# Optimization experiments

Measured on AMD Instinct MI355X. Metric: run time of the kernel, lower is better.

## Reference

```python
import jax, jax.numpy as jnp
import numpy as np

NQ = 8
NL = 3
DIM = 2 ** NQ


def _rx(psi, w, theta):
    # theta: scalar or [B]
    B = psi.shape[0]
    t = jnp.atleast_1d(theta).astype(jnp.float32)
    c = jnp.cos(t / 2)[:, None, None].astype(jnp.complex64)
    s = (-1j * jnp.sin(t / 2))[:, None, None].astype(jnp.complex64)
    p = psi.reshape(B, 2 ** w, 2, -1)
    s0, s1 = p[:, :, 0], p[:, :, 1]
    return jnp.stack([c * s0 + s * s1, s * s0 + c * s1], axis=2).reshape(B, DIM)


def _ry(psi, w, theta):
    B = psi.shape[0]
    t = jnp.atleast_1d(theta).astype(jnp.float32)
    c = jnp.cos(t / 2)[:, None, None].astype(jnp.complex64)
    s = jnp.sin(t / 2)[:, None, None].astype(jnp.complex64)
    p = psi.reshape(B, 2 ** w, 2, -1)
    s0, s1 = p[:, :, 0], p[:, :, 1]
    return jnp.stack([c * s0 - s * s1, s * s0 + c * s1], axis=2).reshape(B, DIM)


def _rz(psi, w, theta):
    B = psi.shape[0]
    t = jnp.atleast_1d(theta).astype(jnp.float32)
    e0 = jnp.exp(-0.5j * t.astype(jnp.complex64))[:, None, None]
    e1 = jnp.exp(0.5j * t.astype(jnp.complex64))[:, None, None]
    p = psi.reshape(B, 2 ** w, 2, -1)
    return jnp.stack([e0 * p[:, :, 0], e1 * p[:, :, 1]], axis=2).reshape(B, DIM)


def _cnot(psi, c, t):
    # control c, target t (wire 0 = most significant axis)
    B = psi.shape[0]
    a, b = (c, t) if c < t else (t, c)
    p = psi.reshape(B, 2 ** a, 2, 2 ** (b - a - 1), 2, -1)
    caxis = 2 if c < t else 4
    taxis = 4 if c < t else 2
    idx = [slice(None)] * 6
    idx[caxis] = 1
    sub = p[tuple(idx)]  # control=1 slab, caxis removed
    fl_axis = taxis - (1 if taxis > caxis else 0)
    p = p.at[tuple(idx)].set(jnp.flip(sub, axis=fl_axis))
    return p.reshape(B, DIM)


# PauliZ signs per wire: [NQ, 2^NQ]
_bits = (np.arange(DIM)[None, :] >> (NQ - 1 - np.arange(NQ)[:, None])) & 1
_Z_SIGNS = jnp.asarray((1 - 2 * _bits).astype(np.float32))


def _quantum_layer(enc, qrx, qry, qrz):
    # enc: [B, NQ] encoding angles; qrx/qry/qrz: [NL, NQ] scalar params
    B = enc.shape[0]
    psi = jnp.zeros((B, DIM), jnp.complex64).at[:, 0].set(1.0)
    for i in range(NQ):
        psi = _rx(psi, i, enc[:, i])
    for l in range(NL):
        for i in range(NQ):
            psi = _rx(psi, i, qrx[l, i])
            psi = _ry(psi, i, qry[l, i])
            psi = _rz(psi, i, qrz[l, i])
        for i in range(NQ - 1):
            psi = _cnot(psi, i, i + 1)
        psi = _cnot(psi, NQ - 1, 0)
    probs = psi.real ** 2 + psi.imag ** 2  # [B, 2^NQ]
    return probs @ _Z_SIGNS.T  # [B, NQ] <Z_i>


def _critic(x, w1, b1, w2, b2, qrx, qry, qrz, w3, b3, w4, b4):
    h = jax.nn.relu(x @ w1 + b1)
    enc = h @ w2 + b2
    ex = _quantum_layer(enc, qrx, qry, qrz)
    h2 = jax.nn.relu(ex @ w3 + b3)
    return h2 @ w4 + b4


def setup_inputs() -> dict:
    key = jax.random.key(0)
    ks = jax.random.split(key, 32)
    B, OBS, ACT, H = 65536, 96, 32, 256
    D = OBS + ACT

    def lin(k, fin, fout):
        return jax.random.normal(k, (fin, fout), jnp.float32) * (1.0 / np.sqrt(fin))

    inp = {
        'state': jax.random.normal(ks[0], (B, OBS), jnp.float32),
        'action': jax.random.normal(ks[1], (B, ACT), jnp.float32),
    }
    for ci, tag in enumerate(['a', 'b']):
        o = 2 + ci * 15
        inp['w1' + tag] = lin(ks[o + 0], D, H)
        inp['b1' + tag] = jnp.zeros((H,), jnp.float32)
        inp['w2' + tag] = lin(ks[o + 1], H, NQ)
        inp['b2' + tag] = jnp.zeros((NQ,), jnp.float32)
        inp['qrx' + tag] = jax.random.normal(ks[o + 2], (NL, NQ), jnp.float32)
        inp['qry' + tag] = jax.random.normal(ks[o + 3], (NL, NQ), jnp.float32)
        inp['qrz' + tag] = jax.random.normal(ks[o + 4], (NL, NQ), jnp.float32)
        inp['w3' + tag] = lin(ks[o + 5], NQ, H)
        inp['b3' + tag] = jnp.zeros((H,), jnp.float32)
        inp['w4' + tag] = lin(ks[o + 6], H, 1)
        inp['b4' + tag] = jnp.zeros((1,), jnp.float32)
    return inp


def reference(state, action,
              w1a, b1a, w2a, b2a, qrxa, qrya, qrza, w3a, b3a, w4a, b4a,
              w1b, b1b, w2b, b2b, qrxb, qryb, qrzb, w3b, b3b, w4b, b4b):
    x = jnp.concatenate([state, action], axis=1)
    q1 = _critic(x, w1a, b1a, w2a, b2a, qrxa, qrya, qrza, w3a, b3a, w4a, b4a)
    q2 = _critic(x, w1b, b1b, w2b, b2b, qrxb, qryb, qrzb, w3b, b3b, w4b, b4b)
    return (q1, q2)
```

## Files before the change

### kernel.cpp

```cpp
#include <hip/hip_runtime.h>
#include <math.h>


typedef __attribute__((ext_vector_type(8))) short bfrag_t;
typedef __attribute__((ext_vector_type(16))) float accv_t;

__device__ __forceinline__ unsigned short f2bf(float x) {
  unsigned u = __float_as_uint(x);
  u += 0x7FFFu + ((u >> 16) & 1u);
  return (unsigned short)(u >> 16);
}
__device__ __forceinline__ float bf2f(unsigned short h) {
  return __uint_as_float(((unsigned)h) << 16);
}
__device__ __forceinline__ unsigned pack2(float a, float b) {
  return (unsigned)f2bf(a) | ((unsigned)f2bf(b) << 16);
}

struct C2 { float r, i; };
__device__ __forceinline__ C2 cmul(C2 a, C2 b){ return C2{a.r*b.r - a.i*b.i, a.r*b.i + a.i*b.r}; }
__device__ __forceinline__ C2 cadd(C2 a, C2 b){ return C2{a.r+b.r, a.i+b.i}; }

#define APPLY2(A,Bx)                                                        \
  { float ar=re[A], ai=im[A], br=re[Bx], bi=im[Bx];                         \
    re[A]  = u00r*ar - u00i*ai + u01r*br - u01i*bi;                         \
    im[A]  = u00r*ai + u00i*ar + u01r*bi + u01i*br;                         \
    re[Bx] = u10r*ar - u10i*ai + u11r*br - u11i*bi;                         \
    im[Bx] = u10r*ai + u10i*ar + u11r*bi + u11i*br; }

__global__ __launch_bounds__(256)
void prep_weights(const float* __restrict__ qrxa, const float* __restrict__ qrya,
                  const float* __restrict__ qrza,
                  const float* __restrict__ qrxb, const float* __restrict__ qryb,
                  const float* __restrict__ qrzb,
                  const float* __restrict__ w1a, const float* __restrict__ w1b,
                  const float* __restrict__ w2a, const float* __restrict__ w2b,
                  const float* __restrict__ w3a, const float* __restrict__ w3b,
                  unsigned short* __restrict__ Bm, unsigned short* __restrict__ Gm,
                  unsigned short* __restrict__ w1p, unsigned short* __restrict__ w2p) {
  int blk = blockIdx.x;
  int tid = threadIdx.x;
  if (blk < 128) {
    __shared__ float sg[192];
    int c = blk >> 6;
    if (tid < 24) {
      const float* qx = c ? qrxb : qrxa;
      const float* qy = c ? qryb : qrya;
      const float* qz = c ? qrzb : qrza;
      int g = tid;
      float tx = 0.5f*qx[g], ty = 0.5f*qy[g], tz = 0.5f*qz[g];
      float cx = cosf(tx), sx = sinf(tx);
      float cy = cosf(ty), sy = sinf(ty);
      float cz = cosf(tz), sz = sinf(tz);
      C2 rx00{cx,0.f}, rx01{0.f,-sx}, rx10{0.f,-sx}, rx11{cx,0.f};
      C2 m00 = cadd(cmul(C2{cy,0.f},rx00), cmul(C2{-sy,0.f},rx10));
      C2 m01 = cadd(cmul(C2{cy,0.f},rx01), cmul(C2{-sy,0.f},rx11));
      C2 m10 = cadd(cmul(C2{sy,0.f},rx00), cmul(C2{cy,0.f},rx10));
      C2 m11 = cadd(cmul(C2{sy,0.f},rx01), cmul(C2{cy,0.f},rx11));
      C2 e0{cz,-sz}, e1{cz,sz};
      C2 u00 = cmul(e0,m00), u01 = cmul(e0,m01), u10 = cmul(e1,m10), u11 = cmul(e1,m11);
      float* o = sg + g*8;
      o[0]=u00.r; o[1]=u00.i; o[2]=u01.r; o[3]=u01.i;
      o[4]=u10.r; o[5]=u10.i; o[6]=u11.r; o[7]=u11.i;
    }
    __syncthreads();
    int lane = tid & 63;
    int wid = blk*4 + (tid >> 6);
    int bcol = wid & 255;
    int p = __popc(bcol) & 3;
    float phr = (p==0) ? 1.f : ((p==2) ? -1.f : 0.f);
    float phi = (p==1) ? -1.f : ((p==3) ? 1.f : 0.f);
    float re[4], im[4];
    #pragma unroll
    for (int j = 0; j < 4; ++j) {
      int idx = 4*lane + j;
      re[j] = (idx==bcol) ? phr : 0.f;
      im[j] = (idx==bcol) ? phi : 0.f;
    }
    #pragma unroll
    for (int l = 0; l < 3; ++l) {
      #pragma unroll
      for (int q = 0; q < 8; ++q) {
        const float* u = &sg[(size_t)(l*8 + q)*8];
        float u00r=u[0],u00i=u[1],u01r=u[2],u01i=u[3];
        float u10r=u[4],u10i=u[5],u11r=u[6],u11i=u[7];
        if (q < 6) {
          int m = 5-q, mask = 1<<m;
          bool s1 = ((lane >> m) & 1) != 0;
          float udr = s1?u11r:u00r, udi = s1?u11i:u00i;
          float uor = s1?u10r:u01r, uoi = s1?u10i:u01i;
          #pragma unroll
          for (int j = 0; j < 4; ++j) {
            float pr = __shfl_xor(re[j], mask);
            float pi = __shfl_xor(im[j], mask);
            float nr = udr*re[j] - udi*im[j] + uor*pr - uoi*pi;
            float ni = udr*im[j] + udi*re[j] + uor*pi + uoi*pr;
            re[j]=nr; im[j]=ni;
          }
        } else if (q == 6) { APPLY2(0,2); APPLY2(1,3); }
        else               { APPLY2(0,1); APPLY2(2,3); }
      }
      #pragma unroll
      for (int cq = 0; cq <= 4; ++cq) {
        int tmask = 1 << (4-cq);
        bool pred = ((lane >> (5-cq)) & 1) != 0;
        #pragma unroll
        for (int j = 0; j < 4; ++j) {
          float sr = __shfl_xor(re[j], tmask);
          float si = __shfl_xor(im[j], tmask);
          re[j] = pred ? sr : re[j];
          im[j] = pred ? si : im[j];
        }
      }
      { bool pred = (lane & 1) != 0;
        float t0, t1;
        t0 = pred?re[2]:re[0]; t1 = pred?re[0]:re[2]; re[0]=t0; re[2]=t1;
        t0 = pred?im[2]:im[0]; t1 = pred?im[0]:im[2]; im[0]=t0; im[2]=t1;
        t0 = pred?re[3]:re[1]; t1 = pred?re[1]:re[3]; re[1]=t0; re[3]=t1;
        t0 = pred?im[3]:im[1]; t1 = pred?im[1]:im[3]; im[1]=t0; im[3]=t1; }
      { float t;
        t=re[2]; re[2]=re[3]; re[3]=t;
        t=im[2]; im[2]=im[3]; im[3]=t; }
      { re[1]=__shfl_xor(re[1],32); im[1]=__shfl_xor(im[1],32);
        re[3]=__shfl_xor(re[3],32); im[3]=__shfl_xor(im[3],32); }
    }
    #pragma unroll
    for (int j = 0; j < 4; ++j) {
      int i = 4*lane + j;
      Bm[(size_t)(c*512 + i)*256 + bcol]       = f2bf(re[j]);
      Bm[(size_t)(c*512 + 256 + i)*256 + bcol] = f2bf(im[j]);
    }
  } else if (blk < 192) {
    int slot = (blk-128)*256 + tid;
    int n = slot & 255, h5 = (slot>>8)&1, ks = (slot>>9)&7, p = (slot>>12)&1, c = slot>>13;
    const float* w1c = c ? w1b : w1a;
    #pragma unroll
    for (int j = 0; j < 8; ++j) {
      float v = w1c[(size_t)(ks*16 + h5*8 + j)*256 + n];
      unsigned short hi = f2bf(v);
      w1p[(size_t)slot*8 + j] = p ? f2bf(v - bf2f(hi)) : hi;
    }
  } else if (blk < 200) {
    int slot = (blk-192)*256 + tid;
    int combo = slot >> 4, part = slot & 15;
    int h5 = combo&1, k16 = (combo>>1)&15, p = (combo>>5)&1, c = (combo>>6)&1;
    const float* w2c = c ? w2b : w2a;
    #pragma unroll
    for (int jj = 0; jj < 16; ++jj) {
      int idx = part*16 + jj;
      int il = idx >> 3, j = idx & 7;
      int n = k16*16 + h5*8 + j;
      float v = (il < 8) ? w2c[(size_t)n*8 + il] : 0.f;
      unsigned short hi = f2bf(v);
      w2p[(size_t)combo*256 + idx] = p ? f2bf(v - bf2f(hi)) : hi;
    }
  } else {
    int idx = (blk-200)*256 + tid;
    int c = idx >> 16, w = (idx >> 13) & 7, ks = (idx >> 9) & 15;
    int l = (idx >> 3) & 63, j = idx & 7;
    int n = 32*w + (l & 31);
    int i = ks*16 + (l >> 5)*8 + j;
    const float* w3 = c ? w3b : w3a;
    float s = 0.f;
    #pragma unroll
    for (int q = 0; q < 8; ++q) {
      float sg2 = ((i >> (7-q)) & 1) ? -1.f : 1.f;
      s += sg2 * w3[q*256 + n];
    }
    Gm[idx] = f2bf(s);
  }
}

__global__ __launch_bounds__(256, 2)
void enc_mfma(const float* __restrict__ state, const float* __restrict__ action,
              const unsigned short* __restrict__ w1p,
              const float* __restrict__ b1a, const float* __restrict__ b1b,
              const unsigned short* __restrict__ w2p,
              const float* __restrict__ b2a, const float* __restrict__ b2b,
              float* __restrict__ enc, int Bn) {
  __shared__ __align__(16) char Bx[2][16384];
  __shared__ __align__(16) float sb1[2][256];
  __shared__ float sb2[2][8];
  __shared__ __align__(16) float encw[4][2][32][8];
  int tid = threadIdx.x;
  int lane = tid & 63, w = tid >> 6, il = lane & 31, h5 = lane >> 5;
  int r0 = blockIdx.x * 64;

  sb1[0][tid] = b1a[tid];
  sb1[1][tid] = b1b[tid];
  if (tid < 8) { sb2[0][tid] = b2a[tid]; sb2[1][tid] = b2b[tid]; }

  {
    int m = tid >> 2, kq = tid & 3;
    const float4* st4 = (const float4*)state;
    const float4* ac4 = (const float4*)action;
    #pragma unroll
    for (int ks = 0; ks < 8; ++ks) {
      float4 v = (ks < 6) ? st4[(size_t)(r0+m)*24 + ks*4 + kq]
                          : ac4[(size_t)(r0+m)*8 + (ks-6)*4 + kq];
      unsigned short hx = f2bf(v.x), hy = f2bf(v.y), hz = f2bf(v.z), hw = f2bf(v.w);
      uint2 hh, ll;
      hh.x = (unsigned)hx | ((unsigned)hy << 16);
      hh.y = (unsigned)hz | ((unsigned)hw << 16);
      ll.x = (unsigned)f2bf(v.x - bf2f(hx)) | ((unsigned)f2bf(v.y - bf2f(hy)) << 16);
      ll.y = (unsigned)f2bf(v.z - bf2f(hz)) | ((unsigned)f2bf(v.w - bf2f(hw)) << 16);
      int off = ks*2048 + m*32 + kq*8;
      *(uint2*)(&Bx[0][off]) = hh;
      *(uint2*)(&Bx[1][off]) = ll;
    }
  }
  __syncthreads();

  for (int c = 0; c < 2; ++c) {
    accv_t A[2][2] = {{{},{}},{{},{}}};
    #pragma unroll
    for (int ks = 0; ks < 8; ++ks) {
      bfrag_t a0h, a0l, a1h, a1l;
      {
        size_t b0 = ((size_t)((c*2+0)*8 + ks)*2 + h5)*256;
        size_t b1 = ((size_t)((c*2+1)*8 + ks)*2 + h5)*256;
        int t0 = 2*w, t1 = 2*w+1;
        a0h = *(const bfrag_t*)(w1p + (b0 + t0*32 + il)*8);
        a0l = *(const bfrag_t*)(w1p + (b1 + t0*32 + il)*8);
        a1h = *(const bfrag_t*)(w1p + (b0 + t1*32 + il)*8);
        a1l = *(const bfrag_t*)(w1p + (b1 + t1*32 + il)*8);
      }
      bfrag_t b0h = *(const bfrag_t*)(&Bx[0][ks*2048 + il*32 + h5*16]);
      bfrag_t b0l = *(const bfrag_t*)(&Bx[1][ks*2048 + il*32 + h5*16]);
      bfrag_t b1h_ = *(const bfrag_t*)(&Bx[0][ks*2048 + (32+il)*32 + h5*16]);
      bfrag_t b1l_ = *(const bfrag_t*)(&Bx[1][ks*2048 + (32+il)*32 + h5*16]);
      A[0][0] = __builtin_amdgcn_mfma_f32_32x32x16_bf16(a0h, b0h, A[0][0], 0,0,0);
      A[0][0] = __builtin_amdgcn_mfma_f32_32x32x16_bf16(a0h, b0l, A[0][0], 0,0,0);
      A[0][0] = __builtin_amdgcn_mfma_f32_32x32x16_bf16(a0l, b0h, A[0][0], 0,0,0);
      A[0][1] = __builtin_amdgcn_mfma_f32_32x32x16_bf16(a0h, b1h_, A[0][1], 0,0,0);
      A[0][1] = __builtin_amdgcn_mfma_f32_32x32x16_bf16(a0h, b1l_, A[0][1], 0,0,0);
      A[0][1] = __builtin_amdgcn_mfma_f32_32x32x16_bf16(a0l, b1h_, A[0][1], 0,0,0);
      A[1][0] = __builtin_amdgcn_mfma_f32_32x32x16_bf16(a1h, b0h, A[1][0], 0,0,0);
      A[1][0] = __builtin_amdgcn_mfma_f32_32x32x16_bf16(a1h, b0l, A[1][0], 0,0,0);
      A[1][0] = __builtin_amdgcn_mfma_f32_32x32x16_bf16(a1l, b0h, A[1][0], 0,0,0);
      A[1][1] = __builtin_amdgcn_mfma_f32_32x32x16_bf16(a1h, b1h_, A[1][1], 0,0,0);
      A[1][1] = __builtin_amdgcn_mfma_f32_32x32x16_bf16(a1h, b1l_, A[1][1], 0,0,0);
      A[1][1] = __builtin_amdgcn_mfma_f32_32x32x16_bf16(a1l, b1h_, A[1][1], 0,0,0);
    }
    #pragma unroll
    for (int nt = 0; nt < 2; ++nt) {
      #pragma unroll
      for (int g = 0; g < 4; ++g) {
        float4 bb = *(const float4*)&sb1[c][(2*w+nt)*32 + 8*g + 4*h5];
        float bba[4] = {bb.x, bb.y, bb.z, bb.w};
        #pragma unroll
        for (int jj = 0; jj < 4; ++jj) {
          A[nt][0][4*g+jj] = fmaxf(A[nt][0][4*g+jj] + bba[jj], 0.f);
          A[nt][1][4*g+jj] = fmaxf(A[nt][1][4*g+jj] + bba[jj], 0.f);
        }
      }
    }
    accv_t Cm[2] = {{},{}};
    #pragma unroll
    for (int k2 = 0; k2 < 4; ++k2) {
      int k16 = 4*w + k2;
      bfrag_t g2h = *(const bfrag_t*)(w2p + ((size_t)((c*2+0)*16 + k16)*2 + h5)*256 + il*8);
      bfrag_t g2l = *(const bfrag_t*)(w2p + ((size_t)((c*2+1)*16 + k16)*2 + h5)*256 + il*8);
      #pragma unroll
      for (int mt = 0; mt < 2; ++mt) {
        unsigned ph[2][2], pl[2][2];
        #pragma unroll
        for (int gi = 0; gi < 2; ++gi) {
          int G = 2*k2 + gi, nt = G >> 2, g = G & 3;
          float f0 = A[nt][mt][4*g+0], f1 = A[nt][mt][4*g+1];
          float f2 = A[nt][mt][4*g+2], f3 = A[nt][mt][4*g+3];
          unsigned short h0 = f2bf(f0), h1 = f2bf(f1), h2 = f2bf(f2), h3 = f2bf(f3);
          ph[gi][0] = (unsigned)h0 | ((unsigned)h1 << 16);
          ph[gi][1] = (unsigned)h2 | ((unsigned)h3 << 16);
          pl[gi][0] = (unsigned)f2bf(f0 - bf2f(h0)) | ((unsigned)f2bf(f1 - bf2f(h1)) << 16);
          pl[gi][1] = (unsigned)f2bf(f2 - bf2f(h2)) | ((unsigned)f2bf(f3 - bf2f(h3)) << 16);
        }
        union { bfrag_t v; unsigned u[4]; } FH, FL;
        #pragma unroll
        for (int r = 0; r < 2; ++r) {
          unsigned own_h = h5 ? ph[1][r] : ph[0][r];
          unsigned alt_h = h5 ? ph[0][r] : ph[1][r];
          unsigned rec_h = __shfl_xor((int)alt_h, 32);
          FH.u[r]   = h5 ? rec_h : own_h;
          FH.u[2+r] = h5 ? own_h : rec_h;
          unsigned own_l = h5 ? pl[1][r] : pl[0][r];
          unsigned alt_l = h5 ? pl[0][r] : pl[1][r];
          unsigned rec_l = __shfl_xor((int)alt_l, 32);
          FL.u[r]   = h5 ? rec_l : own_l;
          FL.u[2+r] = h5 ? own_l : rec_l;
        }
        Cm[mt] = __builtin_amdgcn_mfma_f32_32x32x16_bf16(g2h, FH.v, Cm[mt], 0,0,0);
        Cm[mt] = __builtin_amdgcn_mfma_f32_32x32x16_bf16(g2h, FL.v, Cm[mt], 0,0,0);
        Cm[mt] = __builtin_amdgcn_mfma_f32_32x32x16_bf16(g2l, FH.v, Cm[mt], 0,0,0);
      }
    }
    *(float4*)&encw[w][0][il][4*h5] = make_float4(Cm[0][0], Cm[0][1], Cm[0][2], Cm[0][3]);
    *(float4*)&encw[w][1][il][4*h5] = make_float4(Cm[1][0], Cm[1][1], Cm[1][2], Cm[1][3]);
    __syncthreads();
    #pragma unroll
    for (int half = 0; half < 2; ++half) {
      int s = tid + half*256;
      int e = s & 7, mm = s >> 3;
      float v = sb2[c][e];
      #pragma unroll
      for (int ww = 0; ww < 4; ++ww) v += encw[ww][mm>>5][mm&31][e];
      enc[((size_t)c*Bn + r0 + mm)*8 + e] = v;
    }
    __syncthreads();
  }
}

__global__ __launch_bounds__(512, 2)
void qgemm(const float* __restrict__ enc,
           const unsigned short* __restrict__ Bm, const unsigned short* __restrict__ Gm,
           const float* __restrict__ b3a, const float* __restrict__ w4a, const float* __restrict__ b4a,
           const float* __restrict__ b3b, const float* __restrict__ w4b, const float* __restrict__ b4b,
           float* __restrict__ out, int Bn) {
  __shared__ __align__(16) char APq[33792];
  char* Alds = APq;
  char* Plds = APq + 16896;
  float* qtmp = (float*)APq;

  int tid = threadIdx.x;
  int lane = tid & 63;
  int w = tid >> 6;
  int il = lane & 31;
  int h5 = lane >> 5;

  int c = blockIdx.x >> 8;
  int rowblock = blockIdx.x & 255;
  int rowsPerBlock = Bn >> 8;
  int subtiles = rowsPerBlock >> 5;

  bfrag_t bf0[16], bf1[16];
  {
    const unsigned short* base = Bm + ((size_t)(c*512 + 32*w + il)*256 + h5*8);
    #pragma unroll
    for (int ks = 0; ks < 16; ++ks) {
      bf0[ks] = *(const bfrag_t*)(base + ks*16);
      bf1[ks] = *(const bfrag_t*)(base + 256*256 + ks*16);
    }
  }
  int n2 = 32*w + il;
  const float* b3c = c ? b3b : b3a;
  const float* w4c = c ? w4b : w4a;
  const float* b4c = c ? b4b : b4a;
  float b3v = b3c[n2];
  float w4v = w4c[n2];
  float b4v = b4c[0];
  const unsigned short* Gbase = Gm + ((size_t)(c*8 + w)*16)*512 + lane*8;
  int pwbase = (n2>>4)*1056 + ((n2>>3)&1)*512 + (n2&7)*2;
  int rowAdd = 4*h5;

  int am = tid & 31, ag2 = tid >> 5;
  const float* encb = enc + ((size_t)c*Bn)*8;
  float4 ea, eb;
  {
    const float* ep = encb + (size_t)(rowblock*rowsPerBlock + am)*8;
    ea = *(const float4*)ep;
    eb = *(const float4*)(ep + 4);
  }

  for (int st = 0; st < subtiles; ++st) {
    int r0 = rowblock*rowsPerBlock + st*32;
    __syncthreads();
    {
      float c0,s0,c1,s1,c2,s2,c3,s3,c4,s4,c5,s5,c6,s6,c7,s7;
      __sincosf(0.5f*ea.x, &s0, &c0);
      __sincosf(0.5f*ea.y, &s1, &c1);
      __sincosf(0.5f*ea.z, &s2, &c2);
      __sincosf(0.5f*ea.w, &s3, &c3);
      __sincosf(0.5f*eb.x, &s4, &c4);
      __sincosf(0.5f*eb.y, &s5, &c5);
      __sincosf(0.5f*eb.z, &s6, &c6);
      __sincosf(0.5f*eb.w, &s7, &c7);
      float v0 = (ag2&8) ? s0 : c0;
      float v1 = (ag2&4) ? s1 : c1;
      float v2 = (ag2&2) ? s2 : c2;
      float v3 = (ag2&1) ? s3 : c3;
      float top = v0*v1*v2*v3;
      float hA = top*c4, hB = top*s4;
      float p67[4];
      p67[0] = c6*c7; p67[1] = c6*s7; p67[2] = s6*c7; p67[3] = s6*s7;
      float low[8];
      #pragma unroll
      for (int j = 0; j < 8; ++j) low[j] = ((j&4) ? s5 : c5) * p67[j&3];
      union { bfrag_t v; unsigned u[4]; } pk;
      #pragma unroll
      for (int k = 0; k < 4; ++k) pk.u[k] = pack2(hA*low[2*k], hA*low[2*k+1]);
      *(bfrag_t*)(Alds + ag2*1056 + am*16) = pk.v;
      #pragma unroll
      for (int k = 0; k < 4; ++k) pk.u[k] = pack2(hB*low[2*k], hB*low[2*k+1]);
      *(bfrag_t*)(Alds + ag2*1056 + 512 + am*16) = pk.v;
    }
    __syncthreads();
    if (st + 1 < subtiles) {
      const float* ep = encb + (size_t)(r0 + 32 + am)*8;
      ea = *(const float4*)ep;
      eb = *(const float4*)(ep + 4);
    }
    accv_t acc0 = {}, acc1 = {};
    #pragma unroll
    for (int ks = 0; ks < 16; ++ks) {
      bfrag_t af = *(const bfrag_t*)(Alds + ks*1056 + lane*16);
      acc0 = __builtin_amdgcn_mfma_f32_32x32x16_bf16(af, bf0[ks], acc0, 0, 0, 0);
      acc1 = __builtin_amdgcn_mfma_f32_32x32x16_bf16(af, bf1[ks], acc1, 0, 0, 0);
    }
    #pragma unroll
    for (int r = 0; r < 16; ++r) {
      float P = acc0[r]*acc0[r] + acc1[r]*acc1[r];
      int row = (r&3) + 8*(r>>2) + rowAdd;
      *(unsigned short*)(Plds + pwbase + row*16) = f2bf(P);
    }
    __syncthreads();
    accv_t acc2 = {};
    #pragma unroll 4
    for (int ks = 0; ks < 16; ++ks) {
      bfrag_t pf = *(const bfrag_t*)(Plds + ks*1056 + lane*16);
      bfrag_t gf = *(const bfrag_t*)(Gbase + ks*512);
      acc2 = __builtin_amdgcn_mfma_f32_32x32x16_bf16(pf, gf, acc2, 0, 0, 0);
    }
    float qp[16];
    #pragma unroll
    for (int r = 0; r < 16; ++r) qp[r] = fmaxf(acc2[r] + b3v, 0.f) * w4v;
    __syncthreads();
    #pragma unroll
    for (int r = 0; r < 16; ++r) {
      int row = (r&3) + 8*(r>>2) + rowAdd;
      qtmp[row*256 + n2] = qp[r];
    }
    __syncthreads();
    {
      int row = tid >> 4, seg = tid & 15;
      const float* qrow = qtmp + row*256;
      float s = 0.f;
      #pragma unroll
      for (int j = 0; j < 4; ++j) {
        float4 a = *(const float4*)(qrow + j*64 + seg*4);
        s += (a.x + a.y) + (a.z + a.w);
      }
      s += __shfl_xor(s, 1);
      s += __shfl_xor(s, 2);
      s += __shfl_xor(s, 4);
      s += __shfl_xor(s, 8);
      if (seg == 0) out[(size_t)c*Bn + r0 + row] = s + b4v;
    }
  }
}

extern "C" void kernel_launch(void* const* d_in, const int* in_sizes, int n_in,
                              void* d_out, int out_size, void* d_ws, size_t ws_size,
                              hipStream_t stream) {
  (void)n_in; (void)out_size; (void)ws_size;
  const float* state  = (const float*)d_in[0];
  const float* action = (const float*)d_in[1];
  const float* w1a=(const float*)d_in[2];  const float* b1a=(const float*)d_in[3];
  const float* w2a=(const float*)d_in[4];  const float* b2a=(const float*)d_in[5];
  const float* qrxa=(const float*)d_in[6]; const float* qrya=(const float*)d_in[7];
  const float* qrza=(const float*)d_in[8];
  const float* w3a=(const float*)d_in[9];  const float* b3a=(const float*)d_in[10];
  const float* w4a=(const float*)d_in[11]; const float* b4a=(const float*)d_in[12];
  const float* w1b=(const float*)d_in[13]; const float* b1b=(const float*)d_in[14];
  const float* w2b=(const float*)d_in[15]; const float* b2b=(const float*)d_in[16];
  const float* qrxb=(const float*)d_in[17];const float* qryb=(const float*)d_in[18];
  const float* qrzb=(const float*)d_in[19];
  const float* w3b=(const float*)d_in[20]; const float* b3b=(const float*)d_in[21];
  const float* w4b=(const float*)d_in[22]; const float* b4b=(const float*)d_in[23];

  int B = in_sizes[0] / 96;
  char* wsb = (char*)d_ws;
  unsigned short* Bmat = (unsigned short*)(wsb);
  unsigned short* Gmat = (unsigned short*)(wsb + 524288);
  unsigned short* w1p  = (unsigned short*)(wsb + 786432);
  unsigned short* w2p  = (unsigned short*)(wsb + 1048576);
  float* enc           = (float*)(wsb + 1114112);

  prep_weights<<<712, 256, 0, stream>>>(qrxa,qrya,qrza,qrxb,qryb,qrzb,
                                        w1a,w1b,w2a,w2b,w3a,w3b,
                                        Bmat,Gmat,w1p,w2p);
  enc_mfma<<<B/64, 256, 0, stream>>>(state,action,w1p,b1a,b1b,w2p,b2a,b2b,enc,B);
  qgemm<<<512, 512, 0, stream>>>(enc, Bmat, Gmat, b3a, w4a, b4a, b3b, w4b, b4b,
                                 (float*)d_out, B);
}
```

Before: 229.2 us.

## Process two 32-row subtiles per iteration with double A/P buffers in qgemm

qgemm now handles 64 rows per loop iteration using two A tiles and two P tiles in LDS. The A build for the next pair happens after the second GEMM, and the grid is halved so each block covers twice as many rows. This cuts barriers per row and amortizes the per-block load of the B fragments into registers. LDS use grows to about 129 KB per block, which likely limits occupancy to one block per CU. The A tile row stride also drops its padding (1056 to 1024), which may add bank conflicts.

```diff
diff --git a/kernel.cpp b/kernel.cpp
--- a/kernel.cpp
+++ b/kernel.cpp
@@ -310,16 +310,48 @@
   }
 }
 
+__device__ __forceinline__ void a_build(float4 ea, float4 eb, char* Ab, int ag2, int am) {
+  float c0,s0,c1,s1,c2,s2,c3,s3,c4,s4,c5,s5,c6,s6,c7,s7;
+  __sincosf(0.5f*ea.x, &s0, &c0);
+  __sincosf(0.5f*ea.y, &s1, &c1);
+  __sincosf(0.5f*ea.z, &s2, &c2);
+  __sincosf(0.5f*ea.w, &s3, &c3);
+  __sincosf(0.5f*eb.x, &s4, &c4);
+  __sincosf(0.5f*eb.y, &s5, &c5);
+  __sincosf(0.5f*eb.z, &s6, &c6);
+  __sincosf(0.5f*eb.w, &s7, &c7);
+  float v0 = (ag2&8) ? s0 : c0;
+  float v1 = (ag2&4) ? s1 : c1;
+  float v2 = (ag2&2) ? s2 : c2;
+  float v3 = (ag2&1) ? s3 : c3;
+  float top = v0*v1*v2*v3;
+  float hA = top*c4, hB = top*s4;
+  float p67[4];
+  p67[0] = c6*c7; p67[1] = c6*s7; p67[2] = s6*c7; p67[3] = s6*s7;
+  float low[8];
+  #pragma unroll
+  for (int j = 0; j < 8; ++j) low[j] = ((j&4) ? s5 : c5) * p67[j&3];
+  union { bfrag_t v; unsigned u[4]; } pk;
+  #pragma unroll
+  for (int k = 0; k < 4; ++k) pk.u[k] = pack2(hA*low[2*k], hA*low[2*k+1]);
+  *(bfrag_t*)(Ab + ag2*1024 + am*16) = pk.v;
+  #pragma unroll
+  for (int k = 0; k < 4; ++k) pk.u[k] = pack2(hB*low[2*k], hB*low[2*k+1]);
+  *(bfrag_t*)(Ab + ag2*1024 + 512 + am*16) = pk.v;
+}
+
 __global__ __launch_bounds__(512, 2)
 void qgemm(const float* __restrict__ enc,
            const unsigned short* __restrict__ Bm, const unsigned short* __restrict__ Gm,
            const float* __restrict__ b3a, const float* __restrict__ w4a, const float* __restrict__ b4a,
            const float* __restrict__ b3b, const float* __restrict__ w4b, const float* __restrict__ b4b,
            float* __restrict__ out, int Bn) {
-  __shared__ __align__(16) char APq[33792];
-  char* Alds = APq;
-  char* Plds = APq + 16896;
-  float* qtmp = (float*)APq;
+  __shared__ __align__(16) char APq[132096];
+  char* A0 = APq;
+  char* A1 = APq + 16384;
+  char* P0 = APq + 32768;
+  char* P1 = APq + 49664;
+  float* qtmp = (float*)(APq + 66560);
 
   int tid = threadIdx.x;
   int lane = tid & 63;
@@ -327,10 +359,10 @@
   int il = lane & 31;
   int h5 = lane >> 5;
 
-  int c = blockIdx.x >> 8;
-  int rowblock = blockIdx.x & 255;
-  int rowsPerBlock = Bn >> 8;
-  int subtiles = rowsPerBlock >> 5;
+  int c = blockIdx.x >> 7;
+  int rowblock = blockIdx.x & 127;
+  int rowsPerBlock = Bn >> 7;
+  int npairs = rowsPerBlock >> 6;
 
   bfrag_t bf0[16], bf1[16];
   {
@@ -354,95 +386,91 @@
 
   int am = tid & 31, ag2 = tid >> 5;
   const float* encb = enc + ((size_t)c*Bn)*8;
-  float4 ea, eb;
+  int rbase = rowblock*rowsPerBlock;
+
   {
-    const float* ep = encb + (size_t)(rowblock*rowsPerBlock + am)*8;
-    ea = *(const float4*)ep;
-    eb = *(const float4*)(ep + 4);
+    const float* ep0 = encb + (size_t)(rbase + am)*8;
+    float4 pa0 = *(const float4*)ep0, pb0 = *(const float4*)(ep0 + 4);
+    const float* ep1 = encb + (size_t)(rbase + 32 + am)*8;
+    float4 pa1 = *(const float4*)ep1, pb1 = *(const float4*)(ep1 + 4);
+    a_build(pa0, pb0, A0, ag2, am);
+    a_build(pa1, pb1, A1, ag2, am);
   }
-
-  for (int st = 0; st < subtiles; ++st) {
-    int r0 = rowblock*rowsPerBlock + st*32;
+  __syncthreads();
+
+  for (int st2 = 0; st2 < npairs; ++st2) {
+    int r0 = rbase + st2*64;
+    {
+      accv_t acc0 = {}, acc1 = {};
+      #pragma unroll
+      for (int ks = 0; ks < 16; ++ks) {
+        bfrag_t af = *(const bfrag_t*)(A0 + ks*1024 + lane*16);
+        acc0 = __builtin_amdgcn_mfma_f32_32x32x16_bf16(af, bf0[ks], acc0, 0, 0, 0);
+        acc1 = __builtin_amdgcn_mfma_f32_32x32x16_bf16(af, bf1[ks], acc1, 0, 0, 0);
+      }
+      #pragma unroll
+      for (int r = 0; r < 16; ++r) {
+        float P = acc0[r]*acc0[r] + acc1[r]*acc1[r];
+        int row = (r&3) + 8*(r>>2) + rowAdd;
+        *(unsigned short*)(P0 + pwbase + row*16) = f2bf(P);
+      }
+    }
+    {
+      accv_t acc0 = {}, acc1 = {};
+      #pragma unroll
+      for (int ks = 0; ks < 16; ++ks) {
+        bfrag_t af = *(const bfrag_t*)(A1 + ks*1024 + lane*16);
+        acc0 = __builtin_amdgcn_mfma_f32_32x32x16_bf16(af, bf0[ks], acc0, 0, 0, 0);
+        acc1 = __builtin_amdgcn_mfma_f32_32x32x16_bf16(af, bf1[ks], acc1, 0, 0, 0);
+      }
+      #pragma unroll
+      for (int r = 0; r < 16; ++r) {
+        float P = acc0[r]*acc0[r] + acc1[r]*acc1[r];
+        int row = (r&3) + 8*(r>>2) + rowAdd;
+        *(unsigned short*)(P1 + pwbase + row*16) = f2bf(P);
+      }
+    }
+    __syncthreads();
+    float4 na0, nb0, na1, nb1;
+    bool more = (st2 + 1 < npairs);
+    if (more) {
+      const float* ep0 = encb + (size_t)(r0 + 64 + am)*8;
+      na0 = *(const float4*)ep0; nb0 = *(const float4*)(ep0 + 4);
+      const float* ep1 = encb + (size_t)(r0 + 96 + am)*8;
+      na1 = *(const float4*)ep1; nb1 = *(const float4*)(ep1 + 4);
+    }
+    accv_t acc2a = {}, acc2b = {};
+    #pragma unroll 4
+    for (int ks = 0; ks < 16; ++ks) {
+      bfrag_t gf  = *(const bfrag_t*)(Gbase + ks*512);
+      bfrag_t pf0 = *(const bfrag_t*)(P0 + ks*1056 + lane*16);
+      bfrag_t pf1 = *(const bfrag_t*)(P1 + ks*1056 + lane*16);
+      acc2a = __builtin_amdgcn_mfma_f32_32x32x16_bf16(pf0, gf, acc2a, 0, 0, 0);
+      acc2b = __builtin_amdgcn_mfma_f32_32x32x16_bf16(pf1, gf, acc2b, 0, 0, 0);
+    }
+    #pragma unroll
+    for (int r = 0; r < 16; ++r) {
+      int row = (r&3) + 8*(r>>2) + rowAdd;
+      qtmp[row*256 + n2]        = fmaxf(acc2a[r] + b3v, 0.f) * w4v;
+      qtmp[(32 + row)*256 + n2] = fmaxf(acc2b[r] + b3v, 0.f) * w4v;
+    }
+    if (more) {
+      a_build(na0, nb0, A0, ag2, am);
+      a_build(na1, nb1, A1, ag2, am);
+    }
     __syncthreads();
     {
-      float c0,s0,c1,s1,c2,s2,c3,s3,c4,s4,c5,s5,c6,s6,c7,s7;
-      __sincosf(0.5f*ea.x, &s0, &c0);
-      __sincosf(0.5f*ea.y, &s1, &c1);
-      __sincosf(0.5f*ea.z, &s2, &c2);
-      __sincosf(0.5f*ea.w, &s3, &c3);
-      __sincosf(0.5f*eb.x, &s4, &c4);
-      __sincosf(0.5f*eb.y, &s5, &c5);
-      __sincosf(0.5f*eb.z, &s6, &c6);
-      __sincosf(0.5f*eb.w, &s7, &c7);
-      float v0 = (ag2&8) ? s0 : c0;
-      float v1 = (ag2&4) ? s1 : c1;
-      float v2 = (ag2&2) ? s2 : c2;
-      float v3 = (ag2&1) ? s3 : c3;
-      float top = v0*v1*v2*v3;
-      float hA = top*c4, hB = top*s4;
-      float p67[4];
-      p67[0] = c6*c7; p67[1] = c6*s7; p67[2] = s6*c7; p67[3] = s6*s7;
-      float low[8];
-      #pragma unroll
-      for (int j = 0; j < 8; ++j) low[j] = ((j&4) ? s5 : c5) * p67[j&3];
-      union { bfrag_t v; unsigned u[4]; } pk;
-      #pragma unroll
-      for (int k = 0; k < 4; ++k) pk.u[k] = pack2(hA*low[2*k], hA*low[2*k+1]);
-      *(bfrag_t*)(Alds + ag2*1056 + am*16) = pk.v;
-      #pragma unroll
-      for (int k = 0; k < 4; ++k) pk.u[k] = pack2(hB*low[2*k], hB*low[2*k+1]);
-      *(bfrag_t*)(Alds + ag2*1056 + 512 + am*16) = pk.v;
-    }
-    __syncthreads();
-    if (st + 1 < subtiles) {
-      const float* ep = encb + (size_t)(r0 + 32 + am)*8;
-      ea = *(const float4*)ep;
-      eb = *(const float4*)(ep + 4);
-    }
-    accv_t acc0 = {}, acc1 = {};
-    #pragma unroll
-    for (int ks = 0; ks < 16; ++ks) {
-      bfrag_t af = *(const bfrag_t*)(Alds + ks*1056 + lane*16);
-      acc0 = __builtin_amdgcn_mfma_f32_32x32x16_bf16(af, bf0[ks], acc0, 0, 0, 0);
-      acc1 = __builtin_amdgcn_mfma_f32_32x32x16_bf16(af, bf1[ks], acc1, 0, 0, 0);
-    }
-    #pragma unroll
-    for (int r = 0; r < 16; ++r) {
-      float P = acc0[r]*acc0[r] + acc1[r]*acc1[r];
-      int row = (r&3) + 8*(r>>2) + rowAdd;
-      *(unsigned short*)(Plds + pwbase + row*16) = f2bf(P);
-    }
-    __syncthreads();
-    accv_t acc2 = {};
-    #pragma unroll 4
-    for (int ks = 0; ks < 16; ++ks) {
-      bfrag_t pf = *(const bfrag_t*)(Plds + ks*1056 + lane*16);
-      bfrag_t gf = *(const bfrag_t*)(Gbase + ks*512);
-      acc2 = __builtin_amdgcn_mfma_f32_32x32x16_bf16(pf, gf, acc2, 0, 0, 0);
-    }
-    float qp[16];
-    #pragma unroll
-    for (int r = 0; r < 16; ++r) qp[r] = fmaxf(acc2[r] + b3v, 0.f) * w4v;
-    __syncthreads();
-    #pragma unroll
-    for (int r = 0; r < 16; ++r) {
-      int row = (r&3) + 8*(r>>2) + rowAdd;
-      qtmp[row*256 + n2] = qp[r];
-    }
-    __syncthreads();
-    {
-      int row = tid >> 4, seg = tid & 15;
+      int row = tid >> 3, seg = tid & 7;
       const float* qrow = qtmp + row*256;
       float s = 0.f;
       #pragma unroll
-      for (int j = 0; j < 4; ++j) {
-        float4 a = *(const float4*)(qrow + j*64 + seg*4);
+      for (int t = 0; t < 8; ++t) {
+        float4 a = *(const float4*)(qrow + t*32 + seg*4);
         s += (a.x + a.y) + (a.z + a.w);
       }
       s += __shfl_xor(s, 1);
       s += __shfl_xor(s, 2);
       s += __shfl_xor(s, 4);
-      s += __shfl_xor(s, 8);
       if (seg == 0) out[(size_t)c*Bn + r0 + row] = s + b4v;
     }
   }
@@ -479,6 +507,6 @@
                                         w1a,w1b,w2a,w2b,w3a,w3b,
                                         Bmat,Gmat,w1p,w2p);
   enc_mfma<<<B/64, 256, 0, stream>>>(state,action,w1p,b1a,b1b,w2p,b2a,b2b,enc,B);
-  qgemm<<<512, 512, 0, stream>>>(enc, Bmat, Gmat, b3a, w4a, b4a, b3b, w4b, b4b,
+  qgemm<<<256, 512, 0, stream>>>(enc, Bmat, Gmat, b3a, w4a, b4a, b3b, w4b, b4b,
                                  (float*)d_out, B);
 }
```

Result: faster. 217.5 us (-5.1%).

## Stream B fragments from global, raise occupancy, and separate LDS regions to drop syncs

Applied to the files above, without the earlier changes.

Stops holding the 32 preloaded B-matrix fragments in registers and reloads them from global memory inside the k-loop, which frees registers so launch bounds can ask for 4 blocks per SM instead of 2. LDS grows and gets separate A, P and qtmp regions, so the next subtile's A build can overlap the qtmp write and one barrier per iteration goes away. The padding/strides of P and qtmp are also changed to avoid bank conflicts. The trade-off is repeated global/L2 traffic for the B weights and more LDS per block, which may itself cap occupancy.

```diff
diff --git a/kernel.cpp b/kernel.cpp
--- a/kernel.cpp
+++ b/kernel.cpp
@@ -310,16 +310,46 @@
   }
 }
 
-__global__ __launch_bounds__(512, 2)
+__device__ __forceinline__ void a_build(float4 ea, float4 eb, char* Ab, int ag2, int am) {
+  float c0,s0,c1,s1,c2,s2,c3,s3,c4,s4,c5,s5,c6,s6,c7,s7;
+  __sincosf(0.5f*ea.x, &s0, &c0);
+  __sincosf(0.5f*ea.y, &s1, &c1);
+  __sincosf(0.5f*ea.z, &s2, &c2);
+  __sincosf(0.5f*ea.w, &s3, &c3);
+  __sincosf(0.5f*eb.x, &s4, &c4);
+  __sincosf(0.5f*eb.y, &s5, &c5);
+  __sincosf(0.5f*eb.z, &s6, &c6);
+  __sincosf(0.5f*eb.w, &s7, &c7);
+  float v0 = (ag2&8) ? s0 : c0;
+  float v1 = (ag2&4) ? s1 : c1;
+  float v2 = (ag2&2) ? s2 : c2;
+  float v3 = (ag2&1) ? s3 : c3;
+  float top = v0*v1*v2*v3;
+  float hA = top*c4, hB = top*s4;
+  float p67[4];
+  p67[0] = c6*c7; p67[1] = c6*s7; p67[2] = s6*c7; p67[3] = s6*s7;
+  float low[8];
+  #pragma unroll
+  for (int j = 0; j < 8; ++j) low[j] = ((j&4) ? s5 : c5) * p67[j&3];
+  union { bfrag_t v; unsigned u[4]; } pk;
+  #pragma unroll
+  for (int k = 0; k < 4; ++k) pk.u[k] = pack2(hA*low[2*k], hA*low[2*k+1]);
+  *(bfrag_t*)(Ab + ag2*1024 + am*16) = pk.v;
+  #pragma unroll
+  for (int k = 0; k < 4; ++k) pk.u[k] = pack2(hB*low[2*k], hB*low[2*k+1]);
+  *(bfrag_t*)(Ab + ag2*1024 + 512 + am*16) = pk.v;
+}
+
+__global__ __launch_bounds__(512, 4)
 void qgemm(const float* __restrict__ enc,
            const unsigned short* __restrict__ Bm, const unsigned short* __restrict__ Gm,
            const float* __restrict__ b3a, const float* __restrict__ w4a, const float* __restrict__ b4a,
            const float* __restrict__ b3b, const float* __restrict__ w4b, const float* __restrict__ b4b,
            float* __restrict__ out, int Bn) {
-  __shared__ __align__(16) char APq[33792];
+  __shared__ __align__(16) char APq[66816];
   char* Alds = APq;
-  char* Plds = APq + 16896;
-  float* qtmp = (float*)APq;
+  char* Plds = APq + 16384;
+  float* qtmp = (float*)(APq + 33024);
 
   int tid = threadIdx.x;
   int lane = tid & 63;
@@ -330,17 +360,11 @@
   int c = blockIdx.x >> 8;
   int rowblock = blockIdx.x & 255;
   int rowsPerBlock = Bn >> 8;
-  int subtiles = rowsPerBlock >> 5;
-
-  bfrag_t bf0[16], bf1[16];
-  {
-    const unsigned short* base = Bm + ((size_t)(c*512 + 32*w + il)*256 + h5*8);
-    #pragma unroll
-    for (int ks = 0; ks < 16; ++ks) {
-      bf0[ks] = *(const bfrag_t*)(base + ks*16);
-      bf1[ks] = *(const bfrag_t*)(base + 256*256 + ks*16);
-    }
-  }
+  int nsub = rowsPerBlock >> 5;
+
+  const unsigned short* wb0 = Bm + ((size_t)(c*512 + 32*w + il)*256 + h5*8);
+  const unsigned short* wb1 = wb0 + 256*256;
+
   int n2 = 32*w + il;
   const float* b3c = c ? b3b : b3a;
   const float* w4c = c ? w4b : w4a;
@@ -349,95 +373,66 @@
   float w4v = w4c[n2];
   float b4v = b4c[0];
   const unsigned short* Gbase = Gm + ((size_t)(c*8 + w)*16)*512 + lane*8;
-  int pwbase = (n2>>4)*1056 + ((n2>>3)&1)*512 + (n2&7)*2;
+  int pwbase = (n2>>4)*1040 + ((n2>>3)&1)*528 + (n2&7)*2;
+  int prd = il*16 + h5*528;
   int rowAdd = 4*h5;
 
   int am = tid & 31, ag2 = tid >> 5;
   const float* encb = enc + ((size_t)c*Bn)*8;
-  float4 ea, eb;
+  int rbase = rowblock*rowsPerBlock;
+
   {
-    const float* ep = encb + (size_t)(rowblock*rowsPerBlock + am)*8;
-    ea = *(const float4*)ep;
-    eb = *(const float4*)(ep + 4);
+    const float* ep = encb + (size_t)(rbase + am)*8;
+    float4 pa = *(const float4*)ep, pb = *(const float4*)(ep + 4);
+    a_build(pa, pb, Alds, ag2, am);
   }
-
-  for (int st = 0; st < subtiles; ++st) {
-    int r0 = rowblock*rowsPerBlock + st*32;
+  __syncthreads();
+
+  for (int st = 0; st < nsub; ++st) {
+    int r0 = rbase + st*32;
+    accv_t acc0 = {}, acc1 = {};
+    #pragma unroll 4
+    for (int ks = 0; ks < 16; ++ks) {
+      bfrag_t af = *(const bfrag_t*)(Alds + ks*1024 + lane*16);
+      bfrag_t b0 = *(const bfrag_t*)(wb0 + ks*16);
+      bfrag_t b1 = *(const bfrag_t*)(wb1 + ks*16);
+      acc0 = __builtin_amdgcn_mfma_f32_32x32x16_bf16(af, b0, acc0, 0, 0, 0);
+      acc1 = __builtin_amdgcn_mfma_f32_32x32x16_bf16(af, b1, acc1, 0, 0, 0);
+    }
+    #pragma unroll
+    for (int r = 0; r < 16; ++r) {
+      float Pv = acc0[r]*acc0[r] + acc1[r]*acc1[r];
+      int row = (r&3) + 8*(r>>2) + rowAdd;
+      *(unsigned short*)(Plds + pwbase + row*16) = f2bf(Pv);
+    }
     __syncthreads();
-    {
-      float c0,s0,c1,s1,c2,s2,c3,s3,c4,s4,c5,s5,c6,s6,c7,s7;
-      __sincosf(0.5f*ea.x, &s0, &c0);
-      __sincosf(0.5f*ea.y, &s1, &c1);
-      __sincosf(0.5f*ea.z, &s2, &c2);
-      __sincosf(0.5f*ea.w, &s3, &c3);
-      __sincosf(0.5f*eb.x, &s4, &c4);
-      __sincosf(0.5f*eb.y, &s5, &c5);
-      __sincosf(0.5f*eb.z, &s6, &c6);
-      __sincosf(0.5f*eb.w, &s7, &c7);
-      float v0 = (ag2&8) ? s0 : c0;
-      float v1 = (ag2&4) ? s1 : c1;
-      float v2 = (ag2&2) ? s2 : c2;
-      float v3 = (ag2&1) ? s3 : c3;
-      float top = v0*v1*v2*v3;
-      float hA = top*c4, hB = top*s4;
-      float p67[4];
-      p67[0] = c6*c7; p67[1] = c6*s7; p67[2] = s6*c7; p67[3] = s6*s7;
-      float low[8];
-      #pragma unroll
-      for (int j = 0; j < 8; ++j) low[j] = ((j&4) ? s5 : c5) * p67[j&3];
-      union { bfrag_t v; unsigned u[4]; } pk;
-      #pragma unroll
-      for (int k = 0; k < 4; ++k) pk.u[k] = pack2(hA*low[2*k], hA*low[2*k+1]);
-      *(bfrag_t*)(Alds + ag2*1056 + am*16) = pk.v;
-      #pragma unroll
-      for (int k = 0; k < 4; ++k) pk.u[k] = pack2(hB*low[2*k], hB*low[2*k+1]);
-      *(bfrag_t*)(Alds + ag2*1056 + 512 + am*16) = pk.v;
-    }
-    __syncthreads();
-    if (st + 1 < subtiles) {
+    float4 na, nb;
+    bool more = (st + 1 < nsub);
+    if (more) {
       const float* ep = encb + (size_t)(r0 + 32 + am)*8;
-      ea = *(const float4*)ep;
-      eb = *(const float4*)(ep + 4);
-    }
-    accv_t acc0 = {}, acc1 = {};
-    #pragma unroll
-    for (int ks = 0; ks < 16; ++ks) {
-      bfrag_t af = *(const bfrag_t*)(Alds + ks*1056 + lane*16);
-      acc0 = __builtin_amdgcn_mfma_f32_32x32x16_bf16(af, bf0[ks], acc0, 0, 0, 0);
-      acc1 = __builtin_amdgcn_mfma_f32_32x32x16_bf16(af, bf1[ks], acc1, 0, 0, 0);
-    }
-    #pragma unroll
-    for (int r = 0; r < 16; ++r) {
-      float P = acc0[r]*acc0[r] + acc1[r]*acc1[r];
-      int row = (r&3) + 8*(r>>2) + rowAdd;
-      *(unsigned short*)(Plds + pwbase + row*16) = f2bf(P);
-    }
-    __syncthreads();
+      na = *(const float4*)ep; nb = *(const float4*)(ep + 4);
+    }
     accv_t acc2 = {};
     #pragma unroll 4
     for (int ks = 0; ks < 16; ++ks) {
-      bfrag_t pf = *(const bfrag_t*)(Plds + ks*1056 + lane*16);
       bfrag_t gf = *(const bfrag_t*)(Gbase + ks*512);
+      bfrag_t pf = *(const bfrag_t*)(Plds + ks*1040 + prd);
       acc2 = __builtin_amdgcn_mfma_f32_32x32x16_bf16(pf, gf, acc2, 0, 0, 0);
     }
-    float qp[16];
-    #pragma unroll
-    for (int r = 0; r < 16; ++r) qp[r] = fmaxf(acc2[r] + b3v, 0.f) * w4v;
-    __syncthreads();
     #pragma unroll
     for (int r = 0; r < 16; ++r) {
       int row = (r&3) + 8*(r>>2) + rowAdd;
-      qtmp[row*256 + n2] = qp[r];
-    }
+      qtmp[n2*33 + row] = fmaxf(acc2[r] + b3v, 0.f) * w4v;
+    }
+    if (more) a_build(na, nb, Alds, ag2, am);
     __syncthreads();
     {
       int row = tid >> 4, seg = tid & 15;
-      const float* qrow = qtmp + row*256;
       float s = 0.f;
       #pragma unroll
-      for (int j = 0; j < 4; ++j) {
-        float4 a = *(const float4*)(qrow + j*64 + seg*4);
-        s += (a.x + a.y) + (a.z + a.w);
+      for (int j = 0; j < 16; ++j) {
+        int n = seg*16 + ((j + seg) & 15);
+        s += qtmp[n*33 + row];
       }
       s += __shfl_xor(s, 1);
       s += __shfl_xor(s, 2);
```

New measurement: 292.6 us. 1.28x slower.
